# Kernel tuning notes

Measured on AMD Instinct MI355X. Metric: run time of the kernel, lower is better.

Reference implementation:

```python
import jax, jax.numpy as jnp
import numpy as np

N, E, F_IN, OUT = 10000, 80000, 128, 32
H1, C1 = 8, 256   # conv1: heads=8, out_channels=256, concat=True
H2, C2 = 1, OUT   # conv2: heads=1, out_channels=OUT, concat=False
NEG_SLOPE = 0.2


def _add_self_loops(edge_index, edge_attr, n_nodes):
    # PyG fill_value='mean': self-loop edge_attr = mean of incoming edge attrs per dst node
    src, dst = edge_index[0], edge_index[1]
    s = jax.ops.segment_sum(edge_attr, dst, num_segments=n_nodes)
    cnt = jax.ops.segment_sum(jnp.ones((edge_attr.shape[0],), edge_attr.dtype), dst, num_segments=n_nodes)
    self_attr = s / jnp.maximum(cnt, 1.0)[:, None]
    loop = jnp.arange(n_nodes)
    return (jnp.concatenate([src, loop]), jnp.concatenate([dst, loop]),
            jnp.concatenate([edge_attr, self_attr], axis=0))


def _gatv2(x, src, dst, edge_attr, Wl, bl, Wr, br, We, att, bias, heads, out_ch, concat, n_nodes):
    xl = (x @ Wl + bl).reshape(n_nodes, heads, out_ch)   # source-side projection
    xr = (x @ Wr + br).reshape(n_nodes, heads, out_ch)   # target-side projection
    e = (edge_attr @ We).reshape(-1, heads, out_ch)      # edge feature projection (no bias in PyG)
    m = jax.nn.leaky_relu(xl[src] + xr[dst] + e, NEG_SLOPE)   # [Etot, H, C]
    logits = jnp.einsum('ehc,hc->eh', m, att)            # per-edge attention logits
    # segment softmax over edges grouped by destination node (stable)
    lmax = jax.ops.segment_max(logits, dst, num_segments=n_nodes)
    ex = jnp.exp(logits - lmax[dst])
    denom = jax.ops.segment_sum(ex, dst, num_segments=n_nodes)
    alpha = ex / denom[dst]                              # [Etot, H]
    out = jax.ops.segment_sum(xl[src] * alpha[:, :, None], dst, num_segments=n_nodes)  # [N, H, C]
    out = out.reshape(n_nodes, heads * out_ch) if concat else out.mean(axis=1)
    return out + bias


def setup_inputs() -> dict:
    key = jax.random.key(0)
    ks = jax.random.split(key, 17)
    s = 0.05
    return {
        'x': jax.random.normal(ks[0], (N, F_IN), jnp.float32),
        'edge_index': jax.random.randint(ks[1], (2, E), 0, N),
        'edge_attr': jax.random.normal(ks[2], (E, F_IN), jnp.float32),
        # conv1 params
        'Wl1': jax.random.normal(ks[3], (F_IN, H1 * C1), jnp.float32) * s,
        'bl1': jnp.zeros((H1 * C1,), jnp.float32),
        'Wr1': jax.random.normal(ks[4], (F_IN, H1 * C1), jnp.float32) * s,
        'br1': jnp.zeros((H1 * C1,), jnp.float32),
        'We1': jax.random.normal(ks[5], (F_IN, H1 * C1), jnp.float32) * s,
        'att1': jax.random.normal(ks[6], (H1, C1), jnp.float32) * s,
        'b1': jnp.zeros((H1 * C1,), jnp.float32),
        # conv2 params (input dim = H1*C1 = 2048)
        'Wl2': jax.random.normal(ks[7], (H1 * C1, H2 * C2), jnp.float32) * s,
        'bl2': jnp.zeros((H2 * C2,), jnp.float32),
        'Wr2': jax.random.normal(ks[8], (H1 * C1, H2 * C2), jnp.float32) * s,
        'br2': jnp.zeros((H2 * C2,), jnp.float32),
        'We2': jax.random.normal(ks[9], (F_IN, H2 * C2), jnp.float32) * s,
        'att2': jax.random.normal(ks[10], (H2, C2), jnp.float32) * s,
        'b2': jnp.zeros((C2,), jnp.float32),
    }


def reference(x, edge_index, edge_attr, Wl1, bl1, Wr1, br1, We1, att1, b1,
              Wl2, bl2, Wr2, br2, We2, att2, b2):
    # mode='eval': all dropouts are identity
    src, dst, ea = _add_self_loops(edge_index, edge_attr, N)
    h = _gatv2(x, src, dst, ea, Wl1, bl1, Wr1, br1, We1, att1, b1, H1, C1, True, N)
    h = jax.nn.relu(h)
    out = _gatv2(h, src, dst, ea, Wl2, bl2, Wr2, br2, We2, att2, b2, H2, C2, False, N)
    return jax.nn.relu(out)
```

## Files before the change

kernel.cpp:

```cpp
#include <hip/hip_runtime.h>
#include <hip/hip_bf16.h>

#define N_NODES 10000
#define N_EDGES 80000
#define ETOT (N_EDGES + N_NODES)
#define FD 128
#define D1 2048
#define D2 32
#define NEG 0.2f

typedef __hip_bfloat16 bf16;
typedef __attribute__((ext_vector_type(8))) short short8;
typedef __attribute__((ext_vector_type(4))) short short4v;
typedef __attribute__((ext_vector_type(4))) float f32x4;

__device__ __forceinline__ bf16 f2b(float v){ return __float2bfloat16(v); }
__device__ __forceinline__ short f2bs(float v){ bf16 t=__float2bfloat16(v); return *(short*)&t; }
__device__ __forceinline__ float b2fs(short s){
    return __uint_as_float(((unsigned int)(unsigned short)s) << 16);
}

__global__ void k_deg(const int* __restrict__ ei, int* __restrict__ deg){
    int e = blockIdx.x*256 + threadIdx.x;
    if(e < N_EDGES) atomicAdd(&deg[ei[N_EDGES+e]], 1);
}

__global__ void k_scan(const int* __restrict__ deg, int* __restrict__ row_start){
    __shared__ int sdata[256];
    int tid = threadIdx.x;
    const int CH = 40;
    int base = tid*CH;
    int lsum = 0;
    for(int i=0;i<CH;i++){ int v=base+i; if(v<N_NODES) lsum += deg[v]+1; }
    sdata[tid]=lsum; __syncthreads();
    for(int off=1; off<256; off<<=1){
        int val = (tid>=off)? sdata[tid-off] : 0;
        __syncthreads();
        sdata[tid] += val;
        __syncthreads();
    }
    int run = (tid>0)? sdata[tid-1] : 0;
    for(int i=0;i<CH;i++){
        int v=base+i;
        if(v<=N_NODES){
            row_start[v]=run;
            if(v<N_NODES) run += deg[v]+1;
        }
    }
}

__global__ void k_fill(const int* __restrict__ ei, const int* __restrict__ row_start,
                       int* __restrict__ cursor, int* __restrict__ ecsr,
                       int* __restrict__ srcs, int* __restrict__ dsts){
    int e = blockIdx.x*256 + threadIdx.x;
    if(e >= ETOT) return;
    int src = (e < N_EDGES) ? ei[e]          : (e - N_EDGES);
    int dst = (e < N_EDGES) ? ei[N_EDGES+e]  : (e - N_EDGES);
    int p = atomicAdd(&cursor[dst], 1);
    int pos = row_start[dst]+p;
    ecsr[pos] = e;
    srcs[pos] = src;
    dsts[pos] = dst;
}

__global__ void k_selfmean(const int* __restrict__ ecsr, const int* __restrict__ row_start,
                           const float* __restrict__ ea, float* __restrict__ self_attr){
    int v = blockIdx.x, t = threadIdx.x;
    int start=row_start[v], end=row_start[v+1];
    float s=0.f; int cnt=0;
    for(int i=start;i<end;i++){
        int e=ecsr[i];
        if(e<N_EDGES){ s += ea[(size_t)e*FD+t]; cnt++; }
    }
    self_attr[(size_t)v*FD+t] = s / fmaxf((float)cnt, 1.f);
}

__global__ void k_packAll(const float* __restrict__ We1, const float* __restrict__ Wl1,
                          const float* __restrict__ Wr1, const float* __restrict__ Wl2,
                          const float* __restrict__ Wr2, const float* __restrict__ We2,
                          short* __restrict__ Wb1, short* __restrict__ Wbl1,
                          short* __restrict__ Wbr1, short* __restrict__ Wb2,
                          short* __restrict__ Wb2e){
    int y = blockIdx.y;
    int idx = blockIdx.x*256 + threadIdx.x;
    if(y < 3){
        const float* W = (y==0)? We1 : (y==1)? Wl1 : Wr1;
        short* Wb      = (y==0)? Wb1 : (y==1)? Wbl1 : Wbr1;
        int k = idx >> 11, c = idx & 2047;
        int cb = c>>4, col = c&15, kc = k>>5, quad = (k>>3)&3, j = k&7;
        Wb[((size_t)(cb*4+kc)*64 + quad*16 + col)*8 + j] = f2bs(W[idx]);
    } else {
        if(idx < 131072){
            int k = idx >> 6, c = idx & 63;
            float v = (c < 32) ? Wl2[k*32 + c] : Wr2[k*32 + (c-32)];
            int cb = c>>4, col = c&15, kc = k>>5, quad = (k>>3)&3, j = k&7;
            Wb2[((size_t)(cb*64+kc)*64 + quad*16 + col)*8 + j] = f2bs(v);
        } else if(idx < 131072+4096){
            int t = idx - 131072;
            int k = t >> 5, c = t & 31;
            int cb = c>>4, col = c&15, kc = k>>5, quad = (k>>3)&3, j = k&7;
            Wb2e[((size_t)(cb*4+kc)*64 + quad*16 + col)*8 + j] = f2bs(We2[t]);
        }
    }
}

__global__ __launch_bounds__(256) void k_gemm1m(const float* __restrict__ x,
        const short* __restrict__ Wbl, const float* __restrict__ bl, bf16* __restrict__ outl,
        const short* __restrict__ Wbr, const float* __restrict__ br, bf16* __restrict__ outr){
    const short* Wb   = (blockIdx.y==0)? Wbl : Wbr;
    const float* bias = (blockIdx.y==0)? bl  : br;
    bf16* outp        = (blockIdx.y==0)? outl: outr;
    __shared__ short a_lds[32*128];
    __shared__ float tile[4][32][20];
    int tid = threadIdx.x;
    int r0 = blockIdx.x*32;
    for(int q=tid; q<32*128; q+=256){
        int m=q>>7, k=q&127;
        int gr=r0+m;
        float v = (gr<N_NODES)? x[(size_t)gr*FD+k] : 0.f;
        int kc=k>>5, quad=(k>>3)&3, j=k&7;
        a_lds[((kc*4+quad)*32+m)*8+j] = f2bs(v);
    }
    __syncthreads();
    int w=tid>>6, lane=tid&63, quad=lane>>4, col=lane&15;
    int arow=lane&31, half=lane>>5;
    short8 af[2][4];
    #pragma unroll
    for(int mg=0;mg<2;mg++)
        #pragma unroll
        for(int kc=0;kc<4;kc++)
            af[mg][kc] = *(const short8*)&a_lds[((kc*4+quad)*32+mg*16+col)*8];
    int orow = r0 + arow;
    for(int cbl=0;cbl<32;cbl++){
        int cbg = w*32+cbl;
        f32x4 c0={0,0,0,0}, c1={0,0,0,0};
        #pragma unroll
        for(int kc=0;kc<4;kc++){
            short8 bfr = *(const short8*)(Wb + ((size_t)(cbg*4+kc)*64 + lane)*8);
            c0 = __builtin_amdgcn_mfma_f32_16x16x32_bf16(af[0][kc], bfr, c0, 0,0,0);
            c1 = __builtin_amdgcn_mfma_f32_16x16x32_bf16(af[1][kc], bfr, c1, 0,0,0);
        }
        #pragma unroll
        for(int rg=0;rg<4;rg++){
            tile[w][quad*4+rg][col]    = c0[rg];
            tile[w][16+quad*4+rg][col] = c1[rg];
        }
        int cg = cbg*16 + half*8;
        float4 t0 = *(float4*)&tile[w][arow][half*8];
        float4 t1 = *(float4*)&tile[w][arow][half*8+4];
        float4 b0 = *(const float4*)(bias+cg);
        float4 b1v = *(const float4*)(bias+cg+4);
        if(orow < N_NODES){
            float tv[8]={t0.x,t0.y,t0.z,t0.w,t1.x,t1.y,t1.z,t1.w};
            float bb[8]={b0.x,b0.y,b0.z,b0.w,b1v.x,b1v.y,b1v.z,b1v.w};
            short8 ov;
            #pragma unroll
            for(int j=0;j<8;j++) ov[j] = f2bs(tv[j]+bb[j]);
            *(short8*)(outp + (size_t)orow*D1 + cg) = ov;
        }
    }
}

__global__ __launch_bounds__(256) void k_logit1(const int* __restrict__ ecsr,
        const int* __restrict__ srcs, const int* __restrict__ dsts,
        const float* __restrict__ ea, const float* __restrict__ self_attr,
        const bf16* __restrict__ xl1, const bf16* __restrict__ xr1,
        const short* __restrict__ Wb, const short* __restrict__ Wb2e,
        const float* __restrict__ att1,
        float* __restrict__ logits1p, float* __restrict__ e2){
    __shared__ short a_lds[64*128];
    __shared__ int ssrc[64], sdst[64], sed[64];
    float (*tile)[32][20] = reinterpret_cast<float(*)[32][20]>(a_lds);
    int tid = threadIdx.x;
    int i0 = blockIdx.x*64;
    if(tid<64){
        int i=i0+tid; if(i>=ETOT) i=ETOT-1;
        sed[tid]=ecsr[i]; ssrc[tid]=srcs[i]; sdst[tid]=dsts[i];
    }
    __syncthreads();
    for(int q=tid; q<64*32; q+=256){
        int m=q>>5, kq=(q&31)*4;
        int e=sed[m];
        const float* sp = (e<N_EDGES)? (ea+(size_t)e*FD+kq) : (self_attr+(size_t)(e-N_EDGES)*FD+kq);
        float4 v4 = *(const float4*)sp;
        int kc=kq>>5, quad=(kq>>3)&3, j=kq&7;
        short4v sv; sv[0]=f2bs(v4.x); sv[1]=f2bs(v4.y); sv[2]=f2bs(v4.z); sv[3]=f2bs(v4.w);
        *(short4v*)&a_lds[((kc*4+quad)*64+m)*8+j] = sv;
    }
    __syncthreads();
    int w=tid>>6, lane=tid&63, quad=lane>>4, col=lane&15;
    int arow=lane&31, half=lane>>5;
    short8 af[4][4];
    #pragma unroll
    for(int mg=0;mg<4;mg++)
        #pragma unroll
        for(int kc=0;kc<4;kc++)
            af[mg][kc] = *(const short8*)&a_lds[((kc*4+quad)*64+mg*16+col)*8];
    __syncthreads();
    const bf16* xlpA = xl1 + (size_t)ssrc[arow]*D1;
    const bf16* xrpA = xr1 + (size_t)sdst[arow]*D1;
    const bf16* xlpB = xl1 + (size_t)ssrc[32+arow]*D1;
    const bf16* xrpB = xr1 + (size_t)sdst[32+arow]*D1;
    float acch[4]={0.f,0.f,0.f,0.f};
    for(int cbl=0;cbl<32;cbl++){
        int cbg = w*32+cbl;
        f32x4 c0={0,0,0,0}, c1={0,0,0,0}, c2={0,0,0,0}, c3={0,0,0,0};
        #pragma unroll
        for(int kc=0;kc<4;kc++){
            short8 bfr = *(const short8*)(Wb + ((size_t)(cbg*4+kc)*64 + lane)*8);
            c0 = __builtin_amdgcn_mfma_f32_16x16x32_bf16(af[0][kc], bfr, c0, 0,0,0);
            c1 = __builtin_amdgcn_mfma_f32_16x16x32_bf16(af[1][kc], bfr, c1, 0,0,0);
            c2 = __builtin_amdgcn_mfma_f32_16x16x32_bf16(af[2][kc], bfr, c2, 0,0,0);
            c3 = __builtin_amdgcn_mfma_f32_16x16x32_bf16(af[3][kc], bfr, c3, 0,0,0);
        }
        int hs = cbl>>4;
        int cg = cbg*16 + half*8;
        float4 a0 = *(const float4*)(att1+cg);
        float4 a1 = *(const float4*)(att1+cg+4);
        float av[8]={a0.x,a0.y,a0.z,a0.w,a1.x,a1.y,a1.z,a1.w};
        #pragma unroll
        for(int rg=0;rg<4;rg++){
            tile[w][quad*4+rg][col]    = c0[rg];
            tile[w][16+quad*4+rg][col] = c1[rg];
        }
        {
            float4 t0 = *(float4*)&tile[w][arow][half*8];
            float4 t1 = *(float4*)&tile[w][arow][half*8+4];
            short8 xlv = *(const short8*)(xlpA + cg);
            short8 xrv = *(const short8*)(xrpA + cg);
            float tv[8]={t0.x,t0.y,t0.z,t0.w,t1.x,t1.y,t1.z,t1.w};
            float acc = acch[hs];
            #pragma unroll
            for(int j=0;j<8;j++){
                float m = tv[j] + b2fs(xlv[j]) + b2fs(xrv[j]);
                m = (m>0.f)? m : NEG*m;
                acc += av[j]*m;
            }
            acch[hs] = acc;
        }
        #pragma unroll
        for(int rg=0;rg<4;rg++){
            tile[w][quad*4+rg][col]    = c2[rg];
            tile[w][16+quad*4+rg][col] = c3[rg];
        }
        {
            float4 t0 = *(float4*)&tile[w][arow][half*8];
            float4 t1 = *(float4*)&tile[w][arow][half*8+4];
            short8 xlv = *(const short8*)(xlpB + cg);
            short8 xrv = *(const short8*)(xrpB + cg);
            float tv[8]={t0.x,t0.y,t0.z,t0.w,t1.x,t1.y,t1.z,t1.w};
            float acc = acch[2+hs];
            #pragma unroll
            for(int j=0;j<8;j++){
                float m = tv[j] + b2fs(xlv[j]) + b2fs(xrv[j]);
                m = (m>0.f)? m : NEG*m;
                acc += av[j]*m;
            }
            acch[2+hs] = acc;
        }
    }
    if(w<2){
        f32x4 c0={0,0,0,0}, c1={0,0,0,0}, c2={0,0,0,0}, c3={0,0,0,0};
        #pragma unroll
        for(int kc=0;kc<4;kc++){
            short8 bfr = *(const short8*)(Wb2e + ((size_t)(w*4+kc)*64 + lane)*8);
            c0 = __builtin_amdgcn_mfma_f32_16x16x32_bf16(af[0][kc], bfr, c0, 0,0,0);
            c1 = __builtin_amdgcn_mfma_f32_16x16x32_bf16(af[1][kc], bfr, c1, 0,0,0);
            c2 = __builtin_amdgcn_mfma_f32_16x16x32_bf16(af[2][kc], bfr, c2, 0,0,0);
            c3 = __builtin_amdgcn_mfma_f32_16x16x32_bf16(af[3][kc], bfr, c3, 0,0,0);
        }
        #pragma unroll
        for(int rg=0;rg<4;rg++){
            tile[w][quad*4+rg][col]    = c0[rg];
            tile[w][16+quad*4+rg][col] = c1[rg];
        }
        {
            int i=i0+arow;
            float4 t0 = *(float4*)&tile[w][arow][half*8];
            float4 t1 = *(float4*)&tile[w][arow][half*8+4];
            if(i<ETOT){
                *(float4*)(e2 + (size_t)i*32 + w*16 + half*8)     = t0;
                *(float4*)(e2 + (size_t)i*32 + w*16 + half*8 + 4) = t1;
            }
        }
        #pragma unroll
        for(int rg=0;rg<4;rg++){
            tile[w][quad*4+rg][col]    = c2[rg];
            tile[w][16+quad*4+rg][col] = c3[rg];
        }
        {
            int i=i0+32+arow;
            float4 t0 = *(float4*)&tile[w][arow][half*8];
            float4 t1 = *(float4*)&tile[w][arow][half*8+4];
            if(i<ETOT){
                *(float4*)(e2 + (size_t)i*32 + w*16 + half*8)     = t0;
                *(float4*)(e2 + (size_t)i*32 + w*16 + half*8 + 4) = t1;
            }
        }
    }
    #pragma unroll
    for(int r=0;r<4;r++) acch[r] += __shfl_xor(acch[r],32);
    if(lane<32){
        int iA=i0+arow;
        if(iA<ETOT){
            logits1p[(size_t)iA*8 + w*2  ] = acch[0];
            logits1p[(size_t)iA*8 + w*2+1] = acch[1];
        }
        int iB=i0+32+arow;
        if(iB<ETOT){
            logits1p[(size_t)iB*8 + w*2  ] = acch[2];
            logits1p[(size_t)iB*8 + w*2+1] = acch[3];
        }
    }
}

__global__ void k_agg1(const int* __restrict__ srcs, const int* __restrict__ row_start,
                       const float* __restrict__ logits1p, const bf16* __restrict__ xl1,
                       const float* __restrict__ b1, bf16* __restrict__ hb){
    int tid=threadIdx.x, v=blockIdx.x;
    int start=row_start[v], end=row_start[v+1];
    int w=tid>>6, lane=tid&63;
    int hpar = lane>>5;
    int myc = w*512 + lane*8;
    float ds0=0.f, ds1=0.f;
    for(int i=start+lane;i<end;i+=64){
        float2 lg = *(const float2*)(logits1p + (size_t)i*8 + w*2);
        ds0 += __expf(lg.x);
        ds1 += __expf(lg.y);
    }
    #pragma unroll
    for(int off=32;off>=1;off>>=1){
        ds0 += __shfl_xor(ds0,off);
        ds1 += __shfl_xor(ds1,off);
    }
    float rden = 1.f/((hpar==0)? ds0 : ds1);
    float acc[8]={0,0,0,0,0,0,0,0};
    for(int i=start;i<end;i++){
        int src = srcs[i];
        float2 lg = *(const float2*)(logits1p + (size_t)i*8 + w*2);
        float al = __expf((hpar==0)? lg.x : lg.y) * rden;
        short8 xv = *(const short8*)(xl1 + (size_t)src*D1 + myc);
        #pragma unroll
        for(int j=0;j<8;j++) acc[j] += al*b2fs(xv[j]);
    }
    float4 bb0=*(const float4*)(b1+myc), bb1=*(const float4*)(b1+myc+4);
    float bv[8]={bb0.x,bb0.y,bb0.z,bb0.w,bb1.x,bb1.y,bb1.z,bb1.w};
    short8 ov;
    #pragma unroll
    for(int j=0;j<8;j++) ov[j] = f2bs(fmaxf(acc[j]+bv[j],0.f));
    *(short8*)(hb + (size_t)v*D1 + myc) = ov;
}

__global__ __launch_bounds__(256) void k_gemm2(const bf16* __restrict__ hb,
        const short* __restrict__ Wb2, const float* __restrict__ bl2,
        const float* __restrict__ br2, float* __restrict__ xl2, float* __restrict__ xr2){
    __shared__ float cacc[4][16][64];
    int tid=threadIdx.x, w=tid>>6, lane=tid&63, quad=lane>>4, col=lane&15;
    int r0 = blockIdx.x*16;
    const bf16* hp = hb + (size_t)(r0+col)*D1 + quad*8;
    f32x4 acc[4] = {{0,0,0,0},{0,0,0,0},{0,0,0,0},{0,0,0,0}};
    for(int kc=w*16; kc<w*16+16; kc++){
        short8 af = *(const short8*)(hp + kc*32);
        #pragma unroll
        for(int cb=0;cb<4;cb++){
            short8 bfr = *(const short8*)(Wb2 + ((size_t)(cb*64+kc)*64 + lane)*8);
            acc[cb] = __builtin_amdgcn_mfma_f32_16x16x32_bf16(af, bfr, acc[cb], 0,0,0);
        }
    }
    #pragma unroll
    for(int cb=0;cb<4;cb++)
        #pragma unroll
        for(int rg=0;rg<4;rg++)
            cacc[w][quad*4+rg][cb*16+col] = acc[cb][rg];
    __syncthreads();
    #pragma unroll
    for(int i=0;i<4;i++){
        int idx = tid + 256*i;
        int r = idx>>6, c = idx&63;
        float s = cacc[0][r][c]+cacc[1][r][c]+cacc[2][r][c]+cacc[3][r][c];
        int rr = r0 + r;
        if(c<32) xl2[rr*32+c]      = s + bl2[c];
        else     xr2[rr*32+(c-32)] = s + br2[c-32];
    }
}

__global__ void k_agg2f(const int* __restrict__ srcs, const int* __restrict__ row_start,
                        const float* __restrict__ e2, const float* __restrict__ xl2,
                        const float* __restrict__ xr2, const float* __restrict__ att2,
                        const float* __restrict__ b2v, float* __restrict__ out){
    int tid=threadIdx.x, v=blockIdx.x;
    int start=row_start[v], end=row_start[v+1];
    int le=tid>>5, c=tid&31;
    float xr2v = xr2[v*32+c];
    float attc = att2[c];
    float ds=0.f, acc=0.f;
    for(int i=start+le;i<end;i+=2){
        int src=srcs[i];
        float xlv = xl2[src*32+c];
        float m = e2[(size_t)i*32+c] + xlv + xr2v;
        m = fmaxf(m, NEG*m);
        float p = attc*m;
        #pragma unroll
        for(int off=16;off>=1;off>>=1) p += __shfl_down(p,off,32);
        p = __shfl(p, 0, 32);
        float ep = __expf(p);
        ds  += ep;
        acc += ep*xlv;
    }
    ds  += __shfl_xor(ds,32);
    acc += __shfl_xor(acc,32);
    if(tid<32) out[(size_t)v*D2+c] = fmaxf(acc/ds + b2v[c], 0.f);
}

extern "C" void kernel_launch(void* const* d_in, const int* in_sizes, int n_in,
                              void* d_out, int out_size, void* d_ws, size_t ws_size,
                              hipStream_t stream) {
    const float* x    = (const float*)d_in[0];
    const int*   ei   = (const int*)d_in[1];
    const float* ea   = (const float*)d_in[2];
    const float* Wl1  = (const float*)d_in[3];
    const float* bl1  = (const float*)d_in[4];
    const float* Wr1  = (const float*)d_in[5];
    const float* br1  = (const float*)d_in[6];
    const float* We1  = (const float*)d_in[7];
    const float* att1 = (const float*)d_in[8];
    const float* b1   = (const float*)d_in[9];
    const float* Wl2  = (const float*)d_in[10];
    const float* bl2  = (const float*)d_in[11];
    const float* Wr2  = (const float*)d_in[12];
    const float* br2  = (const float*)d_in[13];
    const float* We2  = (const float*)d_in[14];
    const float* att2 = (const float*)d_in[15];
    const float* b2v  = (const float*)d_in[16];
    float* out = (float*)d_out;

    char* ws = (char*)d_ws;
    size_t off = 0;
    auto alloc = [&](size_t bytes)->char* {
        char* p = ws + off;
        off += (bytes + 255) & ~(size_t)255;
        return p;
    };
    float* self_attr = (float*)alloc((size_t)N_NODES*FD*4);
    int*   deg       = (int*)  alloc((size_t)N_NODES*4);
    int*   cursor    = (int*)  alloc((size_t)N_NODES*4);
    int*   row_start = (int*)  alloc((size_t)(N_NODES+1)*4);
    int*   ecsr      = (int*)  alloc((size_t)ETOT*4);
    int*   srcs      = (int*)  alloc((size_t)ETOT*4);
    int*   dsts      = (int*)  alloc((size_t)ETOT*4);
    float* logits1p  = (float*)alloc((size_t)ETOT*8*4);
    float* e2        = (float*)alloc((size_t)ETOT*32*4);
    bf16*  xl1       = (bf16*) alloc((size_t)N_NODES*D1*2);
    bf16*  xr1       = (bf16*) alloc((size_t)N_NODES*D1*2);
    bf16*  hb        = (bf16*) alloc((size_t)N_NODES*D1*2);
    float* xl2       = (float*)alloc((size_t)N_NODES*D2*4);
    float* xr2       = (float*)alloc((size_t)N_NODES*D2*4);
    short* Wb1       = (short*)alloc((size_t)FD*D1*2);
    short* Wbl1      = (short*)alloc((size_t)FD*D1*2);
    short* Wbr1      = (short*)alloc((size_t)FD*D1*2);
    short* Wb2       = (short*)alloc((size_t)D1*64*2);
    short* Wb2e      = (short*)alloc((size_t)FD*D2*2);
    (void)ws_size; (void)in_sizes; (void)n_in; (void)out_size;

    hipMemsetAsync(deg,    0, (size_t)N_NODES*4, stream);
    hipMemsetAsync(cursor, 0, (size_t)N_NODES*4, stream);

    k_deg<<<(N_EDGES+255)/256, 256, 0, stream>>>(ei, deg);
    k_scan<<<1, 256, 0, stream>>>(deg, row_start);
    k_fill<<<(ETOT+255)/256, 256, 0, stream>>>(ei, row_start, cursor, ecsr, srcs, dsts);
    k_selfmean<<<N_NODES, 128, 0, stream>>>(ecsr, row_start, ea, self_attr);
    dim3 gp(1024, 4);
    k_packAll<<<gp, 256, 0, stream>>>(We1, Wl1, Wr1, Wl2, Wr2, We2,
                                      Wb1, Wbl1, Wbr1, Wb2, Wb2e);

    dim3 g1((N_NODES+31)/32, 2);
    k_gemm1m<<<g1, 256, 0, stream>>>(x, Wbl1, bl1, xl1, Wbr1, br1, xr1);

    k_logit1<<<(ETOT+63)/64, 256, 0, stream>>>(ecsr, srcs, dsts, ea, self_attr,
                                               xl1, xr1, Wb1, Wb2e, att1, logits1p, e2);
    k_agg1<<<N_NODES, 256, 0, stream>>>(srcs, row_start, logits1p, xl1, b1, hb);

    k_gemm2<<<N_NODES/16, 256, 0, stream>>>(hb, Wb2, bl2, br2, xl2, xr2);
    k_agg2f<<<N_NODES, 64, 0, stream>>>(srcs, row_start, e2, xl2, xr2, att2, b2v, out);
}
```

Measured before the change: 426.9 us.

## Software-pipeline MFMA and epilogue in logit kernel; fold cursor reset into scan

In k_logit1 the per-column-block loop is restructured so the MFMA for the next block is issued before the epilogue of the current one. Two accumulator sets alternate, and separate LDS tiles replace the tile that aliased a_lds, which also lets the post-fragment-load barrier go. The aim is to hide MFMA latency and the gathered xl/xr loads behind the leaky-relu and attention math. Separately, the cursor memset is removed and cursor is zeroed inside k_scan, saving one memset launch. The cost is more LDS and more accumulator registers, which may lower occupancy.

```diff
diff --git a/kernel.cpp b/kernel.cpp
--- a/kernel.cpp
+++ b/kernel.cpp
@@ -25,13 +25,17 @@
     if(e < N_EDGES) atomicAdd(&deg[ei[N_EDGES+e]], 1);
 }
 
-__global__ void k_scan(const int* __restrict__ deg, int* __restrict__ row_start){
+__global__ void k_scan(const int* __restrict__ deg, int* __restrict__ row_start,
+                       int* __restrict__ cursor){
     __shared__ int sdata[256];
     int tid = threadIdx.x;
     const int CH = 40;
     int base = tid*CH;
     int lsum = 0;
-    for(int i=0;i<CH;i++){ int v=base+i; if(v<N_NODES) lsum += deg[v]+1; }
+    for(int i=0;i<CH;i++){
+        int v=base+i;
+        if(v<N_NODES){ lsum += deg[v]+1; cursor[v]=0; }
+    }
     sdata[tid]=lsum; __syncthreads();
     for(int off=1; off<256; off<<=1){
         int val = (tid>=off)? sdata[tid-off] : 0;
@@ -169,8 +173,9 @@
         const float* __restrict__ att1,
         float* __restrict__ logits1p, float* __restrict__ e2){
     __shared__ short a_lds[64*128];
+    __shared__ float tileA[4][32][20];
+    __shared__ float tileB[4][32][20];
     __shared__ int ssrc[64], sdst[64], sed[64];
-    float (*tile)[32][20] = reinterpret_cast<float(*)[32][20]>(a_lds);
     int tid = threadIdx.x;
     int i0 = blockIdx.x*64;
     if(tid<64){
@@ -196,36 +201,37 @@
         #pragma unroll
         for(int kc=0;kc<4;kc++)
             af[mg][kc] = *(const short8*)&a_lds[((kc*4+quad)*64+mg*16+col)*8];
-    __syncthreads();
     const bf16* xlpA = xl1 + (size_t)ssrc[arow]*D1;
     const bf16* xrpA = xr1 + (size_t)sdst[arow]*D1;
     const bf16* xlpB = xl1 + (size_t)ssrc[32+arow]*D1;
     const bf16* xrpB = xr1 + (size_t)sdst[32+arow]*D1;
     float acch[4]={0.f,0.f,0.f,0.f};
-    for(int cbl=0;cbl<32;cbl++){
+
+    auto do_mfma = [&](int cbl, f32x4* c){
         int cbg = w*32+cbl;
-        f32x4 c0={0,0,0,0}, c1={0,0,0,0}, c2={0,0,0,0}, c3={0,0,0,0};
         #pragma unroll
         for(int kc=0;kc<4;kc++){
             short8 bfr = *(const short8*)(Wb + ((size_t)(cbg*4+kc)*64 + lane)*8);
-            c0 = __builtin_amdgcn_mfma_f32_16x16x32_bf16(af[0][kc], bfr, c0, 0,0,0);
-            c1 = __builtin_amdgcn_mfma_f32_16x16x32_bf16(af[1][kc], bfr, c1, 0,0,0);
-            c2 = __builtin_amdgcn_mfma_f32_16x16x32_bf16(af[2][kc], bfr, c2, 0,0,0);
-            c3 = __builtin_amdgcn_mfma_f32_16x16x32_bf16(af[3][kc], bfr, c3, 0,0,0);
-        }
+            c[0] = __builtin_amdgcn_mfma_f32_16x16x32_bf16(af[0][kc], bfr, c[0], 0,0,0);
+            c[1] = __builtin_amdgcn_mfma_f32_16x16x32_bf16(af[1][kc], bfr, c[1], 0,0,0);
+            c[2] = __builtin_amdgcn_mfma_f32_16x16x32_bf16(af[2][kc], bfr, c[2], 0,0,0);
+            c[3] = __builtin_amdgcn_mfma_f32_16x16x32_bf16(af[3][kc], bfr, c[3], 0,0,0);
+        }
+    };
+    auto epi = [&](int cbl, f32x4* c){
         int hs = cbl>>4;
-        int cg = cbg*16 + half*8;
+        int cg = (w*32+cbl)*16 + half*8;
         float4 a0 = *(const float4*)(att1+cg);
         float4 a1 = *(const float4*)(att1+cg+4);
         float av[8]={a0.x,a0.y,a0.z,a0.w,a1.x,a1.y,a1.z,a1.w};
         #pragma unroll
         for(int rg=0;rg<4;rg++){
-            tile[w][quad*4+rg][col]    = c0[rg];
-            tile[w][16+quad*4+rg][col] = c1[rg];
+            tileA[w][quad*4+rg][col]    = c[0][rg];
+            tileA[w][16+quad*4+rg][col] = c[1][rg];
         }
         {
-            float4 t0 = *(float4*)&tile[w][arow][half*8];
-            float4 t1 = *(float4*)&tile[w][arow][half*8+4];
+            float4 t0 = *(float4*)&tileA[w][arow][half*8];
+            float4 t1 = *(float4*)&tileA[w][arow][half*8+4];
             short8 xlv = *(const short8*)(xlpA + cg);
             short8 xrv = *(const short8*)(xrpA + cg);
             float tv[8]={t0.x,t0.y,t0.z,t0.w,t1.x,t1.y,t1.z,t1.w};
@@ -240,12 +246,12 @@
         }
         #pragma unroll
         for(int rg=0;rg<4;rg++){
-            tile[w][quad*4+rg][col]    = c2[rg];
-            tile[w][16+quad*4+rg][col] = c3[rg];
+            tileB[w][quad*4+rg][col]    = c[2][rg];
+            tileB[w][16+quad*4+rg][col] = c[3][rg];
         }
         {
-            float4 t0 = *(float4*)&tile[w][arow][half*8];
-            float4 t1 = *(float4*)&tile[w][arow][half*8+4];
+            float4 t0 = *(float4*)&tileB[w][arow][half*8];
+            float4 t1 = *(float4*)&tileB[w][arow][half*8+4];
             short8 xlv = *(const short8*)(xlpB + cg);
             short8 xrv = *(const short8*)(xrpB + cg);
             float tv[8]={t0.x,t0.y,t0.z,t0.w,t1.x,t1.y,t1.z,t1.w};
@@ -258,6 +264,21 @@
             }
             acch[2+hs] = acc;
         }
+    };
+
+    f32x4 cA[4], cB[4];
+    #pragma unroll
+    for(int r=0;r<4;r++) cA[r]=(f32x4){0,0,0,0};
+    do_mfma(0, cA);
+    for(int cbl=0; cbl<32; cbl+=2){
+        #pragma unroll
+        for(int r=0;r<4;r++) cB[r]=(f32x4){0,0,0,0};
+        do_mfma(cbl+1, cB);
+        epi(cbl, cA);
+        #pragma unroll
+        for(int r=0;r<4;r++) cA[r]=(f32x4){0,0,0,0};
+        if(cbl+2<32) do_mfma(cbl+2, cA);
+        epi(cbl+1, cB);
     }
     if(w<2){
         f32x4 c0={0,0,0,0}, c1={0,0,0,0}, c2={0,0,0,0}, c3={0,0,0,0};
@@ -271,13 +292,13 @@
         }
         #pragma unroll
         for(int rg=0;rg<4;rg++){
-            tile[w][quad*4+rg][col]    = c0[rg];
-            tile[w][16+quad*4+rg][col] = c1[rg];
+            tileA[w][quad*4+rg][col]    = c0[rg];
+            tileA[w][16+quad*4+rg][col] = c1[rg];
         }
         {
             int i=i0+arow;
-            float4 t0 = *(float4*)&tile[w][arow][half*8];
-            float4 t1 = *(float4*)&tile[w][arow][half*8+4];
+            float4 t0 = *(float4*)&tileA[w][arow][half*8];
+            float4 t1 = *(float4*)&tileA[w][arow][half*8+4];
             if(i<ETOT){
                 *(float4*)(e2 + (size_t)i*32 + w*16 + half*8)     = t0;
                 *(float4*)(e2 + (size_t)i*32 + w*16 + half*8 + 4) = t1;
@@ -285,13 +306,13 @@
         }
         #pragma unroll
         for(int rg=0;rg<4;rg++){
-            tile[w][quad*4+rg][col]    = c2[rg];
-            tile[w][16+quad*4+rg][col] = c3[rg];
+            tileB[w][quad*4+rg][col]    = c2[rg];
+            tileB[w][16+quad*4+rg][col] = c3[rg];
         }
         {
             int i=i0+32+arow;
-            float4 t0 = *(float4*)&tile[w][arow][half*8];
-            float4 t1 = *(float4*)&tile[w][arow][half*8+4];
+            float4 t0 = *(float4*)&tileB[w][arow][half*8];
+            float4 t1 = *(float4*)&tileB[w][arow][half*8+4];
             if(i<ETOT){
                 *(float4*)(e2 + (size_t)i*32 + w*16 + half*8)     = t0;
                 *(float4*)(e2 + (size_t)i*32 + w*16 + half*8 + 4) = t1;
@@ -462,11 +483,10 @@
     short* Wb2e      = (short*)alloc((size_t)FD*D2*2);
     (void)ws_size; (void)in_sizes; (void)n_in; (void)out_size;
 
-    hipMemsetAsync(deg,    0, (size_t)N_NODES*4, stream);
-    hipMemsetAsync(cursor, 0, (size_t)N_NODES*4, stream);
+    hipMemsetAsync(deg, 0, (size_t)N_NODES*4, stream);
 
     k_deg<<<(N_EDGES+255)/256, 256, 0, stream>>>(ei, deg);
-    k_scan<<<1, 256, 0, stream>>>(deg, row_start);
+    k_scan<<<1, 256, 0, stream>>>(deg, row_start, cursor);
     k_fill<<<(ETOT+255)/256, 256, 0, stream>>>(ei, row_start, cursor, ecsr, srcs, dsts);
     k_selfmean<<<N_NODES, 128, 0, stream>>>(ecsr, row_start, ea, self_attr);
     dim3 gp(1024, 4);
```

After: 440.5 us. +3.2%, slower.

## Double gemm1 row tile, fold cursor memset into scan, split logit1 tile LDS

Applied to the files above, without the earlier changes.

The node-projection GEMM now handles 64 rows per block instead of 32. Each weight fragment loaded from global memory feeds four MFMAs instead of two, and the x staging uses float4 loads. The cursor zeroing moves from a separate memset into the scan kernel, removing one launch. In k_logit1 the epilogue tile gets its own shared array instead of aliasing a_lds, so one __syncthreads can be dropped, at the cost of more LDS per block and fewer gemm blocks.

```diff
diff --git a/kernel.cpp b/kernel.cpp
--- a/kernel.cpp
+++ b/kernel.cpp
@@ -25,13 +25,17 @@
     if(e < N_EDGES) atomicAdd(&deg[ei[N_EDGES+e]], 1);
 }
 
-__global__ void k_scan(const int* __restrict__ deg, int* __restrict__ row_start){
+__global__ void k_scan(const int* __restrict__ deg, int* __restrict__ row_start,
+                       int* __restrict__ cursor){
     __shared__ int sdata[256];
     int tid = threadIdx.x;
     const int CH = 40;
     int base = tid*CH;
     int lsum = 0;
-    for(int i=0;i<CH;i++){ int v=base+i; if(v<N_NODES) lsum += deg[v]+1; }
+    for(int i=0;i<CH;i++){
+        int v=base+i;
+        if(v<N_NODES){ lsum += deg[v]+1; cursor[v]=0; }
+    }
     sdata[tid]=lsum; __syncthreads();
     for(int off=1; off<256; off<<=1){
         int val = (tid>=off)? sdata[tid-off] : 0;
@@ -110,53 +114,76 @@
     const short* Wb   = (blockIdx.y==0)? Wbl : Wbr;
     const float* bias = (blockIdx.y==0)? bl  : br;
     bf16* outp        = (blockIdx.y==0)? outl: outr;
-    __shared__ short a_lds[32*128];
+    __shared__ short a_lds[64*128];
     __shared__ float tile[4][32][20];
     int tid = threadIdx.x;
-    int r0 = blockIdx.x*32;
-    for(int q=tid; q<32*128; q+=256){
-        int m=q>>7, k=q&127;
+    int r0 = blockIdx.x*64;
+    for(int q=tid; q<64*32; q+=256){
+        int m=q>>5, kq=(q&31)*4;
         int gr=r0+m;
-        float v = (gr<N_NODES)? x[(size_t)gr*FD+k] : 0.f;
-        int kc=k>>5, quad=(k>>3)&3, j=k&7;
-        a_lds[((kc*4+quad)*32+m)*8+j] = f2bs(v);
+        float4 v4 = {0,0,0,0};
+        if(gr<N_NODES) v4 = *(const float4*)(x+(size_t)gr*FD+kq);
+        int kc=kq>>5, quad=(kq>>3)&3, j=kq&7;
+        short4v sv; sv[0]=f2bs(v4.x); sv[1]=f2bs(v4.y); sv[2]=f2bs(v4.z); sv[3]=f2bs(v4.w);
+        *(short4v*)&a_lds[((kc*4+quad)*64+m)*8+j] = sv;
     }
     __syncthreads();
     int w=tid>>6, lane=tid&63, quad=lane>>4, col=lane&15;
     int arow=lane&31, half=lane>>5;
-    short8 af[2][4];
-    #pragma unroll
-    for(int mg=0;mg<2;mg++)
+    short8 af[4][4];
+    #pragma unroll
+    for(int mg=0;mg<4;mg++)
         #pragma unroll
         for(int kc=0;kc<4;kc++)
-            af[mg][kc] = *(const short8*)&a_lds[((kc*4+quad)*32+mg*16+col)*8];
-    int orow = r0 + arow;
+            af[mg][kc] = *(const short8*)&a_lds[((kc*4+quad)*64+mg*16+col)*8];
+    int orowA = r0 + arow;
+    int orowB = r0 + 32 + arow;
     for(int cbl=0;cbl<32;cbl++){
         int cbg = w*32+cbl;
-        f32x4 c0={0,0,0,0}, c1={0,0,0,0};
+        f32x4 c0={0,0,0,0}, c1={0,0,0,0}, c2={0,0,0,0}, c3={0,0,0,0};
         #pragma unroll
         for(int kc=0;kc<4;kc++){
             short8 bfr = *(const short8*)(Wb + ((size_t)(cbg*4+kc)*64 + lane)*8);
             c0 = __builtin_amdgcn_mfma_f32_16x16x32_bf16(af[0][kc], bfr, c0, 0,0,0);
             c1 = __builtin_amdgcn_mfma_f32_16x16x32_bf16(af[1][kc], bfr, c1, 0,0,0);
-        }
+            c2 = __builtin_amdgcn_mfma_f32_16x16x32_bf16(af[2][kc], bfr, c2, 0,0,0);
+            c3 = __builtin_amdgcn_mfma_f32_16x16x32_bf16(af[3][kc], bfr, c3, 0,0,0);
+        }
+        int cg = cbg*16 + half*8;
+        float4 b0 = *(const float4*)(bias+cg);
+        float4 b1v = *(const float4*)(bias+cg+4);
+        float bb[8]={b0.x,b0.y,b0.z,b0.w,b1v.x,b1v.y,b1v.z,b1v.w};
         #pragma unroll
         for(int rg=0;rg<4;rg++){
             tile[w][quad*4+rg][col]    = c0[rg];
             tile[w][16+quad*4+rg][col] = c1[rg];
         }
-        int cg = cbg*16 + half*8;
-        float4 t0 = *(float4*)&tile[w][arow][half*8];
-        float4 t1 = *(float4*)&tile[w][arow][half*8+4];
-        float4 b0 = *(const float4*)(bias+cg);
-        float4 b1v = *(const float4*)(bias+cg+4);
-        if(orow < N_NODES){
-            float tv[8]={t0.x,t0.y,t0.z,t0.w,t1.x,t1.y,t1.z,t1.w};
-            float bb[8]={b0.x,b0.y,b0.z,b0.w,b1v.x,b1v.y,b1v.z,b1v.w};
-            short8 ov;
-            #pragma unroll
-            for(int j=0;j<8;j++) ov[j] = f2bs(tv[j]+bb[j]);
-            *(short8*)(outp + (size_t)orow*D1 + cg) = ov;
+        {
+            float4 t0 = *(float4*)&tile[w][arow][half*8];
+            float4 t1 = *(float4*)&tile[w][arow][half*8+4];
+            if(orowA < N_NODES){
+                float tv[8]={t0.x,t0.y,t0.z,t0.w,t1.x,t1.y,t1.z,t1.w};
+                short8 ov;
+                #pragma unroll
+                for(int j=0;j<8;j++) ov[j] = f2bs(tv[j]+bb[j]);
+                *(short8*)(outp + (size_t)orowA*D1 + cg) = ov;
+            }
+        }
+        #pragma unroll
+        for(int rg=0;rg<4;rg++){
+            tile[w][quad*4+rg][col]    = c2[rg];
+            tile[w][16+quad*4+rg][col] = c3[rg];
+        }
+        {
+            float4 t0 = *(float4*)&tile[w][arow][half*8];
+            float4 t1 = *(float4*)&tile[w][arow][half*8+4];
+            if(orowB < N_NODES){
+                float tv[8]={t0.x,t0.y,t0.z,t0.w,t1.x,t1.y,t1.z,t1.w};
+                short8 ov;
+                #pragma unroll
+                for(int j=0;j<8;j++) ov[j] = f2bs(tv[j]+bb[j]);
+                *(short8*)(outp + (size_t)orowB*D1 + cg) = ov;
+            }
         }
     }
 }
@@ -169,8 +196,8 @@
         const float* __restrict__ att1,
         float* __restrict__ logits1p, float* __restrict__ e2){
     __shared__ short a_lds[64*128];
+    __shared__ float tile[4][32][20];
     __shared__ int ssrc[64], sdst[64], sed[64];
-    float (*tile)[32][20] = reinterpret_cast<float(*)[32][20]>(a_lds);
     int tid = threadIdx.x;
     int i0 = blockIdx.x*64;
     if(tid<64){
@@ -196,7 +223,6 @@
         #pragma unroll
         for(int kc=0;kc<4;kc++)
             af[mg][kc] = *(const short8*)&a_lds[((kc*4+quad)*64+mg*16+col)*8];
-    __syncthreads();
     const bf16* xlpA = xl1 + (size_t)ssrc[arow]*D1;
     const bf16* xrpA = xr1 + (size_t)sdst[arow]*D1;
     const bf16* xlpB = xl1 + (size_t)ssrc[32+arow]*D1;
@@ -462,18 +488,17 @@
     short* Wb2e      = (short*)alloc((size_t)FD*D2*2);
     (void)ws_size; (void)in_sizes; (void)n_in; (void)out_size;
 
-    hipMemsetAsync(deg,    0, (size_t)N_NODES*4, stream);
-    hipMemsetAsync(cursor, 0, (size_t)N_NODES*4, stream);
+    hipMemsetAsync(deg, 0, (size_t)N_NODES*4, stream);
 
     k_deg<<<(N_EDGES+255)/256, 256, 0, stream>>>(ei, deg);
-    k_scan<<<1, 256, 0, stream>>>(deg, row_start);
+    k_scan<<<1, 256, 0, stream>>>(deg, row_start, cursor);
     k_fill<<<(ETOT+255)/256, 256, 0, stream>>>(ei, row_start, cursor, ecsr, srcs, dsts);
     k_selfmean<<<N_NODES, 128, 0, stream>>>(ecsr, row_start, ea, self_attr);
     dim3 gp(1024, 4);
     k_packAll<<<gp, 256, 0, stream>>>(We1, Wl1, Wr1, Wl2, Wr2, We2,
                                       Wb1, Wbl1, Wbr1, Wb2, Wb2e);
 
-    dim3 g1((N_NODES+31)/32, 2);
+    dim3 g1((N_NODES+63)/64, 2);
     k_gemm1m<<<g1, 256, 0, stream>>>(x, Wbl1, bl1, xl1, Wbr1, br1, xr1);
 
     k_logit1<<<(ETOT+63)/64, 256, 0, stream>>>(ecsr, srcs, dsts, ea, self_attr,
```

Result: no change. 422.8 us (-1.0%).
